# Performance work log

Hardware: AMD Instinct MI355X
Metric: run time of the kernel (lower is better)

## Reference

```python
import jax, jax.numpy as jnp
import numpy as np

NUM_CENTROIDS = 2048
EMA_DECAY = 0.99
GAMMA = 1.0
EPS = 1e-08


def setup_inputs() -> dict:
    key = jax.random.key(0)
    k1, k2 = jax.random.split(key)
    B, T, D = 32, 512, 512
    inputs = jax.random.normal(k1, (B, T, D), dtype=jnp.float32)
    # variance_scaling(0.1, 'fan_avg', 'normal') init for the codebook
    fan_avg = (NUM_CENTROIDS + D) / 2.0
    std = np.sqrt(0.1 / fan_avg).astype(np.float32)
    codebook = jax.random.normal(k2, (NUM_CENTROIDS, D), dtype=jnp.float32) * std
    cluster_counts = jnp.ones((NUM_CENTROIDS,), dtype=jnp.float32)
    return {"inputs": inputs, "codebook": codebook,
            "cluster_counts": cluster_counts, "train": 1}


def reference(inputs, codebook, cluster_counts, train):
    D = inputs.shape[-1]
    K = codebook.shape[0]
    flat = jnp.reshape(inputs, (-1, D))  # [N, D]

    # similarity of stop-gradient features to codebook rows: [N, K]
    features = jax.lax.stop_gradient(flat)
    similarity = jnp.einsum('nd,kd->nk', features, codebook)
    scores = jax.nn.softmax(similarity, axis=-1)
    nn_idx = jnp.argmax(scores, axis=-1)  # [N]

    # cluster counts = column sums of one-hot encodings -> scatter-add
    counts = jnp.zeros((K,), dtype=scores.dtype).at[nn_idx].add(1.0)
    if train:
        new_counts = EMA_DECAY * cluster_counts + (1.0 - EMA_DECAY) * counts
    else:
        new_counts = cluster_counts

    # one_hot @ codebook == gather of codebook rows
    quantized = codebook[nn_idx]  # [N, D]
    quantized = quantized - jnp.mean(quantized, axis=-1, keepdims=True)
    quantized = quantized / jnp.linalg.norm(quantized, axis=-1, keepdims=True)
    quantized = jnp.reshape(quantized, inputs.shape)

    # entropy-based quantization loss (scalar), broadcast to [..., K]
    h_clust = -jnp.mean(jnp.sum(scores * jnp.log2(scores + EPS), axis=-1))
    diversity = jnp.mean(scores, axis=0)
    h_diversity = -jnp.sum(diversity * jnp.log2(diversity + EPS))
    loss = h_clust - GAMMA * h_diversity
    quantization_loss = jnp.full(inputs.shape[:-1] + (K,), loss)

    # straight-through estimator
    quantized = inputs + jax.lax.stop_gradient(quantized - inputs)

    nn_idx_out = jnp.reshape(nn_idx, inputs.shape[:-1])[None]  # [1, B, T]
    codebook_values = jax.lax.stop_gradient(codebook)[None]     # [1, K, D]
    return (quantized, quantization_loss, nn_idx_out, codebook_values, new_counts)
```

## Files before the change

### kernel.cpp

```cpp
#include <hip/hip_runtime.h>
#include <cstddef>
#include <cmath>

#define NROWS 16384
#define DIM   512
#define KC    2048

#define Q_OFF    0ul
#define LOSS_OFF 8388608ul
#define NN_OFF   41943040ul
#define CB_OFF   41959424ul
#define CNT_OFF  43008000ul

#define ENT_OFF  4194304ul

#define FLAG_CAP 4096
#define FLAG_TAU 3e-5f

#define WS_LOSS   0
#define WS_CNT    4
#define WS_NFLAG  3076
#define WS_FLAGS  3080
#define WS_DIVLOG 15376

typedef __attribute__((ext_vector_type(8))) short short8;
typedef __attribute__((ext_vector_type(4))) float f32x4;

__device__ __forceinline__ short hi1(float f) {
    return (short)(__float_as_uint(f) >> 16);
}
__device__ __forceinline__ short lo1(float f) {
    unsigned int u = __float_as_uint(f);
    float l = f - __uint_as_float(u & 0xffff0000u);
    return (short)(__float_as_uint(l) >> 16);
}
__device__ __forceinline__ short8 hi8(float4 a, float4 b) {
    short8 r;
    r[0]=hi1(a.x); r[1]=hi1(a.y); r[2]=hi1(a.z); r[3]=hi1(a.w);
    r[4]=hi1(b.x); r[5]=hi1(b.y); r[6]=hi1(b.z); r[7]=hi1(b.w);
    return r;
}
__device__ __forceinline__ short8 lo8(float4 a, float4 b) {
    short8 r;
    r[0]=lo1(a.x); r[1]=lo1(a.y); r[2]=lo1(a.z); r[3]=lo1(a.w);
    r[4]=lo1(b.x); r[5]=lo1(b.y); r[6]=lo1(b.z); r[7]=lo1(b.w);
    return r;
}

__global__ __launch_bounds__(256) void convsplit(const float* __restrict__ x,
                                                 const float* __restrict__ cb,
                                                 ushort* __restrict__ ah,
                                                 ushort* __restrict__ al,
                                                 ushort* __restrict__ bh,
                                                 ushort* __restrict__ bl,
                                                 int* __restrict__ ws) {
    if (blockIdx.x == 0) {
        for (int j = threadIdx.x + WS_CNT; j < WS_CNT + 2048; j += 256) ws[j] = 0;
        if (threadIdx.x == 0) ws[WS_NFLAG] = 0;
    }
    size_t i = (size_t)blockIdx.x * 256 + threadIdx.x;
    const float* src; ushort* dh; ushort* dl; size_t off;
    if (i < 1048576ul) {
        src = x;  dh = ah; dl = al; off = i * 8;
    } else {
        src = cb; dh = bh; dl = bl; off = (i - 1048576ul) * 8;
    }
    float4 a = *(const float4*)(src + off);
    float4 b = *(const float4*)(src + off + 4);
    *(short8*)(dh + off) = hi8(a, b);
    *(short8*)(dl + off) = lo8(a, b);
}

#define P_AH 0
#define P_AL 8192
#define P_BH 16384
#define P_BL 24576
#define BUFS 32768

__global__ __launch_bounds__(512, 2) void gemm_mfma(const ushort* __restrict__ Ah,
                                                    const ushort* __restrict__ Al,
                                                    const ushort* __restrict__ Bh,
                                                    const ushort* __restrict__ Bl,
                                                    float* __restrict__ C) {
    __shared__ ushort smem[65536];
    const int t    = threadIdx.x;
    const int n0   = blockIdx.x * 256;
    const int m0   = blockIdx.y * 256;
    const int lane = t & 63, quad = lane >> 4, lr = lane & 15;
    const int w = t >> 6, wm = w >> 2, wn = w & 3;
    const int wb = w * 1024;

    f32x4 acc[8][4] = {};

    const int srow = w * 32 + (lane >> 2);
    const int gc   = (((lane & 3) ^ ((lane >> 3) & 3)) << 3);

    const ushort* gAh0 = Ah + (size_t)(m0 + srow) * DIM + gc;
    const ushort* gAh1 = gAh0 + 16 * DIM;
    const ushort* gAl0 = Al + (size_t)(m0 + srow) * DIM + gc;
    const ushort* gAl1 = gAl0 + 16 * DIM;
    const ushort* gBh0 = Bh + (size_t)(n0 + srow) * DIM + gc;
    const ushort* gBh1 = gBh0 + 16 * DIM;
    const ushort* gBl0 = Bl + (size_t)(n0 + srow) * DIM + gc;
    const ushort* gBl1 = gBl0 + 16 * DIM;

    const int swz   = ((quad ^ ((lr >> 1) & 3)) << 3);
    const int raOff = (wm * 128 + lr) * 32 + swz;
    const int rbOff = (wn * 64  + lr) * 32 + swz;

    #define GLD16(G, LOFF)                                                          \
        __builtin_amdgcn_global_load_lds(                                           \
            (const __attribute__((address_space(1))) unsigned int*)(G),             \
            (__attribute__((address_space(3))) unsigned int*)(smem + (LOFF)), 16, 0, 0)

    GLD16(gAh0, P_AH + wb);
    GLD16(gAh1, P_AH + wb + 512);
    GLD16(gBh0, P_BH + wb);
    GLD16(gBh1, P_BH + wb + 512);
    GLD16(gAl0, P_AL + wb);
    GLD16(gAl1, P_AL + wb + 512);
    GLD16(gBl0, P_BL + wb);
    GLD16(gBl1, P_BL + wb + 512);
    asm volatile("s_waitcnt vmcnt(4)" ::: "memory");
    __builtin_amdgcn_s_barrier();
    __builtin_amdgcn_sched_barrier(0);

    short8 ah[8], bb[4], al[8], bl[4];

    #pragma unroll 1
    for (int kk = 0; kk < 15; ++kk) {
        const int cb  = (kk & 1) * BUFS;
        const int nb  = cb ^ BUFS;
        const int k0n = (kk + 1) * 32;

        #pragma unroll
        for (int mt = 0; mt < 8; ++mt) ah[mt] = *(const short8*)(smem + cb + P_AH + raOff + mt * 512);
        #pragma unroll
        for (int nt = 0; nt < 4; ++nt) bb[nt] = *(const short8*)(smem + cb + P_BH + rbOff + nt * 512);
        GLD16(gAh0 + k0n, nb + P_AH + wb);
        GLD16(gAh1 + k0n, nb + P_AH + wb + 512);
        GLD16(gBh0 + k0n, nb + P_BH + wb);
        asm volatile("s_waitcnt vmcnt(5)" ::: "memory");
        __builtin_amdgcn_s_barrier();
        __builtin_amdgcn_sched_barrier(0);
        __builtin_amdgcn_s_setprio(1);
        #pragma unroll
        for (int mt = 0; mt < 8; ++mt)
            #pragma unroll
            for (int nt = 0; nt < 4; ++nt)
                acc[mt][nt] = __builtin_amdgcn_mfma_f32_16x16x32_bf16(ah[mt], bb[nt], acc[mt][nt], 0, 0, 0);
        __builtin_amdgcn_s_setprio(0);
        __builtin_amdgcn_s_barrier();
        __builtin_amdgcn_sched_barrier(0);

        #pragma unroll
        for (int mt = 0; mt < 8; ++mt) al[mt] = *(const short8*)(smem + cb + P_AL + raOff + mt * 512);
        GLD16(gBh1 + k0n, nb + P_BH + wb + 512);
        GLD16(gAl0 + k0n, nb + P_AL + wb);
        GLD16(gAl1 + k0n, nb + P_AL + wb + 512);
        asm volatile("s_waitcnt vmcnt(6)" ::: "memory");
        __builtin_amdgcn_s_barrier();
        __builtin_amdgcn_sched_barrier(0);
        __builtin_amdgcn_s_setprio(1);
        #pragma unroll
        for (int mt = 0; mt < 8; ++mt)
            #pragma unroll
            for (int nt = 0; nt < 4; ++nt)
                acc[mt][nt] = __builtin_amdgcn_mfma_f32_16x16x32_bf16(al[mt], bb[nt], acc[mt][nt], 0, 0, 0);
        __builtin_amdgcn_s_setprio(0);
        __builtin_amdgcn_s_barrier();
        __builtin_amdgcn_sched_barrier(0);

        #pragma unroll
        for (int nt = 0; nt < 4; ++nt) bl[nt] = *(const short8*)(smem + cb + P_BL + rbOff + nt * 512);
        GLD16(gBl0 + k0n, nb + P_BL + wb);
        GLD16(gBl1 + k0n, nb + P_BL + wb + 512);
        asm volatile("s_waitcnt vmcnt(4)" ::: "memory");
        __builtin_amdgcn_s_barrier();
        __builtin_amdgcn_sched_barrier(0);
        __builtin_amdgcn_s_setprio(1);
        #pragma unroll
        for (int mt = 0; mt < 8; ++mt)
            #pragma unroll
            for (int nt = 0; nt < 4; ++nt)
                acc[mt][nt] = __builtin_amdgcn_mfma_f32_16x16x32_bf16(ah[mt], bl[nt], acc[mt][nt], 0, 0, 0);
        __builtin_amdgcn_s_setprio(0);
        __builtin_amdgcn_s_barrier();
        __builtin_amdgcn_sched_barrier(0);
    }

    {
        const int cb = BUFS;
        #pragma unroll
        for (int mt = 0; mt < 8; ++mt) ah[mt] = *(const short8*)(smem + cb + P_AH + raOff + mt * 512);
        #pragma unroll
        for (int nt = 0; nt < 4; ++nt) bb[nt] = *(const short8*)(smem + cb + P_BH + rbOff + nt * 512);
        asm volatile("s_waitcnt vmcnt(2)" ::: "memory");
        __builtin_amdgcn_s_barrier();
        __builtin_amdgcn_sched_barrier(0);
        #pragma unroll
        for (int mt = 0; mt < 8; ++mt)
            #pragma unroll
            for (int nt = 0; nt < 4; ++nt)
                acc[mt][nt] = __builtin_amdgcn_mfma_f32_16x16x32_bf16(ah[mt], bb[nt], acc[mt][nt], 0, 0, 0);
        __builtin_amdgcn_s_barrier();
        __builtin_amdgcn_sched_barrier(0);

        #pragma unroll
        for (int mt = 0; mt < 8; ++mt) al[mt] = *(const short8*)(smem + cb + P_AL + raOff + mt * 512);
        asm volatile("s_waitcnt vmcnt(0)" ::: "memory");
        __builtin_amdgcn_s_barrier();
        __builtin_amdgcn_sched_barrier(0);
        #pragma unroll
        for (int mt = 0; mt < 8; ++mt)
            #pragma unroll
            for (int nt = 0; nt < 4; ++nt)
                acc[mt][nt] = __builtin_amdgcn_mfma_f32_16x16x32_bf16(al[mt], bb[nt], acc[mt][nt], 0, 0, 0);
        __builtin_amdgcn_s_barrier();
        __builtin_amdgcn_sched_barrier(0);

        #pragma unroll
        for (int nt = 0; nt < 4; ++nt) bl[nt] = *(const short8*)(smem + cb + P_BL + rbOff + nt * 512);
        #pragma unroll
        for (int mt = 0; mt < 8; ++mt)
            #pragma unroll
            for (int nt = 0; nt < 4; ++nt)
                acc[mt][nt] = __builtin_amdgcn_mfma_f32_16x16x32_bf16(ah[mt], bl[nt], acc[mt][nt], 0, 0, 0);
    }
    #undef GLD16

    #pragma unroll
    for (int mt = 0; mt < 8; ++mt) {
        #pragma unroll
        for (int nt = 0; nt < 4; ++nt) {
            const int r0 = m0 + wm * 128 + mt * 16 + quad * 4;
            const int c0 = n0 + wn * 64 + nt * 16 + lr;
            #pragma unroll
            for (int j = 0; j < 4; ++j)
                C[(size_t)(r0 + j) * KC + c0] = acc[mt][nt][j];
        }
    }
}

__device__ __forceinline__ float block_reduce_sum(float v, volatile float* sf,
                                                  int lane, int w) {
    #pragma unroll
    for (int off = 32; off; off >>= 1) v += __shfl_xor(v, off, 64);
    if (lane == 0) sf[w] = v;
    __syncthreads();
    v = sf[0] + sf[1] + sf[2] + sf[3];
    __syncthreads();
    return v;
}

__global__ __launch_bounds__(256, 4) void rowpass(const float* __restrict__ sim,
                                                  float* __restrict__ nn,
                                                  float* __restrict__ divpart2,
                                                  int*   __restrict__ counts,
                                                  float* __restrict__ entpart,
                                                  int*   __restrict__ nflag,
                                                  int*   __restrict__ flags) {
    __shared__ float divp[KC];
    __shared__ float sent[4];
    const int t = threadIdx.x, lane = t & 63, w = t >> 6;
    const int b = blockIdx.x;
    const int row0 = b * 8 + w * 2;
    const int col0 = lane << 2;

    float4 dacc[8] = {};
    float ent_acc = 0.f;
    const float* base = sim + (size_t)row0 * KC + col0;

    #pragma unroll 1
    for (int rr = 0; rr < 2; ++rr) {
        float4 cur[8];
        const float* rp = base + (size_t)rr * KC;
        #pragma unroll
        for (int j = 0; j < 8; ++j) cur[j] = *(const float4*)(rp + 256 * j);

        float bv = -3.0e38f, rv = -3.0e38f;
        int   bi = 0x7fffffff, ri = 0x7fffffff;
        #pragma unroll
        for (int j = 0; j < 8; ++j) {
            #pragma unroll
            for (int c = 0; c < 4; ++c) {
                float v = (&cur[j].x)[c];
                int   i = col0 + c + 256 * j;
                if (v > bv || (v == bv && i < bi)) { rv = bv; ri = bi; bv = v; bi = i; }
                else if (v > rv || (v == rv && i < ri)) { rv = v; ri = i; }
            }
        }
        #pragma unroll
        for (int off = 32; off; off >>= 1) {
            float obv = __shfl_xor(bv, off, 64);
            int   obi = __shfl_xor(bi, off, 64);
            float orv = __shfl_xor(rv, off, 64);
            int   ori = __shfl_xor(ri, off, 64);
            bool ob = (obv > bv) || (obv == bv && obi < bi);
            float c1v = ob ? bv : obv;  int c1i = ob ? bi : obi;
            float c2v = ob ? orv : rv;  int c2i = ob ? ori : ri;
            bv = ob ? obv : bv;  bi = ob ? obi : bi;
            bool rb = (c1v > c2v) || (c1v == c2v && c1i < c2i);
            rv = rb ? c1v : c2v;  ri = rb ? c1i : c2i;
        }
        const float m = bv;

        float Z = 0.f, S = 0.f;
        #pragma unroll
        for (int j = 0; j < 8; ++j) {
            #pragma unroll
            for (int c = 0; c < 4; ++c) {
                float d = (&cur[j].x)[c] - m;
                float e = expf(d);
                Z += e; S += e * d;
                (&cur[j].x)[c] = e;
            }
        }
        #pragma unroll
        for (int off = 32; off; off >>= 1) {
            Z += __shfl_xor(Z, off, 64);
            S += __shfl_xor(S, off, 64);
        }
        const float inv = 1.0f / Z;
        #pragma unroll
        for (int j = 0; j < 8; ++j) {
            dacc[j].x += cur[j].x * inv; dacc[j].y += cur[j].y * inv;
            dacc[j].z += cur[j].z * inv; dacc[j].w += cur[j].w * inv;
        }

        if (lane == 0) {
            ent_acc += 1.4426950408889634f * (S * inv) - log2f(Z) + 2.9546393e-5f;
            atomicAdd(&counts[bi], 1);
            nn[row0 + rr] = (float)bi;
            if (bv - rv < FLAG_TAU) {
                int e = atomicAdd(nflag, 1);
                if (e < FLAG_CAP) {
                    flags[3*e] = row0 + rr; flags[3*e+1] = bi; flags[3*e+2] = ri;
                }
            }
        }
    }

    if (lane == 0) sent[w] = ent_acc;
    for (int ww = 0; ww < 4; ++ww) {
        if (w == ww) {
            #pragma unroll
            for (int j = 0; j < 8; ++j) {
                float4* p = (float4*)&divp[col0 + 256 * j];
                if (ww == 0) *p = dacc[j];
                else {
                    float4 v = *p;
                    v.x += dacc[j].x; v.y += dacc[j].y;
                    v.z += dacc[j].z; v.w += dacc[j].w;
                    *p = v;
                }
            }
        }
        __syncthreads();
    }
    float4* dst = (float4*)(divpart2 + (size_t)b * KC);
    dst[t]       = *(float4*)&divp[t * 4];
    dst[t + 256] = *(float4*)&divp[t * 4 + 1024];
    if (t == 0) entpart[b] = sent[0] + sent[1] + sent[2] + sent[3];
}

__global__ __launch_bounds__(256) void fixfin(const float* __restrict__ divpart2,
                                              float* __restrict__ part2,
                                              const float* __restrict__ A,
                                              const float* __restrict__ B,
                                              float* __restrict__ nn,
                                              int*   __restrict__ counts,
                                              const int* __restrict__ flags,
                                              const int* __restrict__ nflagp) {
    const int t = threadIdx.x;
    if (blockIdx.x < 128) {
        const int b = blockIdx.x;
        const float* dp = divpart2 + (size_t)b * 16 * KC;
        #pragma unroll
        for (int j = 0; j < 8; ++j) {
            int c = t + 256 * j;
            float s = 0.f;
            #pragma unroll
            for (int r = 0; r < 16; ++r) s += dp[(size_t)r * KC + c];
            part2[(size_t)b * KC + c] = s;
        }
    } else {
        __shared__ float sf[4];
        int nf = *nflagp; if (nf > FLAG_CAP) nf = FLAG_CAP;
        const int lane = t & 63, w = t >> 6;
        for (int e = blockIdx.x - 128; e < nf; e += 128) {
            const int row = flags[3*e], i1 = flags[3*e+1], i2 = flags[3*e+2];
            const float* ar = A + (size_t)row * DIM;
            const float* b1 = B + (size_t)i1 * DIM;
            const float* b2 = B + (size_t)i2 * DIM;
            float d1 = ar[t] * b1[t] + ar[t + 256] * b1[t + 256];
            float d2 = ar[t] * b2[t] + ar[t + 256] * b2[t + 256];
            d1 = block_reduce_sum(d1, sf, lane, w);
            d2 = block_reduce_sum(d2, sf, lane, w);
            if (t == 0 && (d2 > d1 || (d2 == d1 && i2 < i1))) {
                nn[row] = (float)i2;
                atomicSub(&counts[i1], 1);
                atomicAdd(&counts[i2], 1);
            }
            __syncthreads();
        }
    }
}

__global__ __launch_bounds__(256) void fin1b(const float* __restrict__ part2,
                                             float* __restrict__ divlog8) {
    __shared__ float sf[4];
    const int t = threadIdx.x, lane = t & 63, w = t >> 6;
    const int c = blockIdx.x * 256 + t;
    float s = 0.f;
    for (int r = 0; r < 128; ++r) s += part2[(size_t)r * KC + c];
    float d = s * (1.0f / 16384.0f);
    float v = d * log2f(d + 1e-8f);
    float S = block_reduce_sum(v, sf, lane, w);
    if (t == 0) divlog8[blockIdx.x] = S;
}

__global__ __launch_bounds__(256) void fin2(const float* __restrict__ entpart,
                                            const float* __restrict__ divlog8,
                                            float* __restrict__ lossp) {
    __shared__ float sf[4];
    const int t = threadIdx.x, lane = t & 63, w = t >> 6;
    float se = 0.f;
    #pragma unroll
    for (int k = 0; k < 8; ++k) se += entpart[t + 256 * k];
    float Se = block_reduce_sum(se, sf, lane, w);
    float Sd = block_reduce_sum((t < 8) ? divlog8[t] : 0.f, sf, lane, w);
    if (t == 0)
        lossp[0] = (float)(-(double)Se / 16384.0 + (double)Sd);
}

__global__ __launch_bounds__(256) void tail(const float* __restrict__ x,
                                            const float* __restrict__ cb,
                                            const float* __restrict__ oldc,
                                            const int*   __restrict__ counts,
                                            const float* __restrict__ lossp,
                                            const int*   __restrict__ train,
                                            const float* __restrict__ nn,
                                            float* __restrict__ out) {
    const int bb = blockIdx.x;
    const int t  = threadIdx.x;
    if (bb < 4096) {
        const int lane = t & 63;
        const int row  = (bb << 2) + (t >> 6);
        const int idx  = (int)nn[row];
        const float* c  = cb + (size_t)idx * DIM;
        const float* xr = x  + (size_t)row * DIM;

        float4 q0 = *(const float4*)(c + lane * 8);
        float4 q1 = *(const float4*)(c + lane * 8 + 4);

        float s = q0.x+q0.y+q0.z+q0.w + q1.x+q1.y+q1.z+q1.w;
        #pragma unroll
        for (int off = 32; off; off >>= 1) s += __shfl_xor(s, off, 64);
        const float mean = s * (1.0f / 512.0f);
        q0.x -= mean; q0.y -= mean; q0.z -= mean; q0.w -= mean;
        q1.x -= mean; q1.y -= mean; q1.z -= mean; q1.w -= mean;

        float ss = q0.x*q0.x+q0.y*q0.y+q0.z*q0.z+q0.w*q0.w
                 + q1.x*q1.x+q1.y*q1.y+q1.z*q1.z+q1.w*q1.w;
        #pragma unroll
        for (int off = 32; off; off >>= 1) ss += __shfl_xor(ss, off, 64);
        const float inv = 1.0f / sqrtf(ss);

        float4 x0 = *(const float4*)(xr + lane * 8);
        float4 x1 = *(const float4*)(xr + lane * 8 + 4);
        float4 o0, o1;
        o0.x = x0.x + (q0.x*inv - x0.x); o0.y = x0.y + (q0.y*inv - x0.y);
        o0.z = x0.z + (q0.z*inv - x0.z); o0.w = x0.w + (q0.w*inv - x0.w);
        o1.x = x1.x + (q1.x*inv - x1.x); o1.y = x1.y + (q1.y*inv - x1.y);
        o1.z = x1.z + (q1.z*inv - x1.z); o1.w = x1.w + (q1.w*inv - x1.w);
        *(float4*)(out + (size_t)row * DIM + lane * 8)     = o0;
        *(float4*)(out + (size_t)row * DIM + lane * 8 + 4) = o1;
    } else {
        const int bb2 = bb - 4096;
        if (bb2 < 8192) {
            const float l = lossp[0];
            const float4 v = make_float4(l, l, l, l);
            float4* lo = (float4*)(out + LOSS_OFF);
            size_t base4 = (size_t)bb2 * 1024 + t;
            lo[base4]       = v;
            lo[base4 + 256] = v;
            lo[base4 + 512] = v;
            lo[base4 + 768] = v;
        } else if (bb2 < 8192 + 1024) {
            size_t j = (size_t)(bb2 - 8192) * 256 + t;
            ((float4*)(out + CB_OFF))[j] = ((const float4*)cb)[j];
        } else {
            int k = (bb2 - 9216) * 256 + t;
            float nc = train[0] ? 0.99f * oldc[k] + 0.01f * (float)counts[k]
                                : oldc[k];
            out[CNT_OFF + k] = nc;
        }
    }
}

extern "C" void kernel_launch(void* const* d_in, const int* in_sizes, int n_in,
                              void* d_out, int out_size, void* d_ws, size_t ws_size,
                              hipStream_t stream) {
    const float* x     = (const float*)d_in[0];
    const float* cb    = (const float*)d_in[1];
    const float* oldc  = (const float*)d_in[2];
    const int*   train = (const int*)d_in[3];
    float* out = (float*)d_out;

    float* sim      = out + LOSS_OFF;
    float* divpart2 = out + Q_OFF;
    float* entpart  = out + Q_OFF + ENT_OFF;
    float* part2    = out + CB_OFF;
    float* nn       = out + NN_OFF;

    ushort* Ah = (ushort*)(out + Q_OFF);
    ushort* Al = Ah + 8388608ul;
    ushort* Bh = (ushort*)(out + CB_OFF);
    ushort* Bl = Bh + 1048576ul;

    float* lossp   = (float*)d_ws + WS_LOSS;
    int*   counts  = (int*)d_ws   + WS_CNT;
    int*   nflag   = (int*)d_ws   + WS_NFLAG;
    int*   flags   = (int*)d_ws   + WS_FLAGS;
    float* divlog8 = (float*)d_ws + WS_DIVLOG;

    convsplit<<<4608, 256, 0, stream>>>(x, cb, Ah, Al, Bh, Bl, (int*)d_ws);
    gemm_mfma<<<dim3(KC / 256, NROWS / 256), 512, 0, stream>>>(Ah, Al, Bh, Bl, sim);
    rowpass<<<2048, 256, 0, stream>>>(sim, nn, divpart2, counts, entpart, nflag, flags);
    fixfin<<<256, 256, 0, stream>>>(divpart2, part2, x, cb, nn, counts, flags, nflag);
    fin1b<<<8, 256, 0, stream>>>(part2, divlog8);
    fin2<<<1, 256, 0, stream>>>(entpart, divlog8, lossp);
    tail<<<4096 + 9224, 256, 0, stream>>>(x, cb, oldc, counts, lossp, train, nn, out);
}
```

Before: 354.1 us.

## Restructure GEMM k-loop to issue full next-stage prefetch then one barrier per step

Replaces the three-phase interleaved prefetch/compute schedule, which had a barrier between each phase, with a simpler double-buffered loop. Each iteration issues all eight async global-to-LDS loads for the next k-step, waits for the current buffer, runs one barrier, reads all fragments, and then runs all three MFMA groups back to back. The intent is to cut barrier count and sync overhead per k-step and to fold the peeled final iteration into the loop. In exchange, global loads are no longer interleaved with the MFMA groups inside a step, more fragment registers are live at once, and a trailing barrier is still needed before the buffer is reused.

```diff
diff --git a/kernel.cpp b/kernel.cpp
--- a/kernel.cpp
+++ b/kernel.cpp
@@ -113,72 +113,57 @@
             (const __attribute__((address_space(1))) unsigned int*)(G),             \
             (__attribute__((address_space(3))) unsigned int*)(smem + (LOFF)), 16, 0, 0)
 
-    GLD16(gAh0, P_AH + wb);
-    GLD16(gAh1, P_AH + wb + 512);
-    GLD16(gBh0, P_BH + wb);
-    GLD16(gBh1, P_BH + wb + 512);
-    GLD16(gAl0, P_AL + wb);
-    GLD16(gAl1, P_AL + wb + 512);
-    GLD16(gBl0, P_BL + wb);
-    GLD16(gBl1, P_BL + wb + 512);
-    asm volatile("s_waitcnt vmcnt(4)" ::: "memory");
-    __builtin_amdgcn_s_barrier();
-    __builtin_amdgcn_sched_barrier(0);
+    #define ISSUE8(k0v, nbv)                                                        \
+        do {                                                                        \
+            GLD16(gAh0 + (k0v), (nbv) + P_AH + wb);                                 \
+            GLD16(gAh1 + (k0v), (nbv) + P_AH + wb + 512);                           \
+            GLD16(gBh0 + (k0v), (nbv) + P_BH + wb);                                 \
+            GLD16(gBh1 + (k0v), (nbv) + P_BH + wb + 512);                           \
+            GLD16(gAl0 + (k0v), (nbv) + P_AL + wb);                                 \
+            GLD16(gAl1 + (k0v), (nbv) + P_AL + wb + 512);                           \
+            GLD16(gBl0 + (k0v), (nbv) + P_BL + wb);                                 \
+            GLD16(gBl1 + (k0v), (nbv) + P_BL + wb + 512);                           \
+        } while (0)
+
+    ISSUE8(0, 0);
 
     short8 ah[8], bb[4], al[8], bl[4];
 
     #pragma unroll 1
-    for (int kk = 0; kk < 15; ++kk) {
-        const int cb  = (kk & 1) * BUFS;
-        const int nb  = cb ^ BUFS;
-        const int k0n = (kk + 1) * 32;
-
-        #pragma unroll
-        for (int mt = 0; mt < 8; ++mt) ah[mt] = *(const short8*)(smem + cb + P_AH + raOff + mt * 512);
-        #pragma unroll
-        for (int nt = 0; nt < 4; ++nt) bb[nt] = *(const short8*)(smem + cb + P_BH + rbOff + nt * 512);
-        GLD16(gAh0 + k0n, nb + P_AH + wb);
-        GLD16(gAh1 + k0n, nb + P_AH + wb + 512);
-        GLD16(gBh0 + k0n, nb + P_BH + wb);
-        asm volatile("s_waitcnt vmcnt(5)" ::: "memory");
+    for (int kk = 0; kk < 16; ++kk) {
+        const int cb = (kk & 1) * BUFS;
+
+        if (kk < 15) {
+            const int nb  = cb ^ BUFS;
+            const int k0n = (kk + 1) * 32;
+            ISSUE8(k0n, nb);
+            asm volatile("s_waitcnt vmcnt(8)" ::: "memory");
+        } else {
+            asm volatile("s_waitcnt vmcnt(0)" ::: "memory");
+        }
         __builtin_amdgcn_s_barrier();
         __builtin_amdgcn_sched_barrier(0);
+
+        #pragma unroll
+        for (int mt = 0; mt < 8; ++mt) ah[mt] = *(const short8*)(smem + cb + P_AH + raOff + mt * 512);
+        #pragma unroll
+        for (int nt = 0; nt < 4; ++nt) bb[nt] = *(const short8*)(smem + cb + P_BH + rbOff + nt * 512);
+        #pragma unroll
+        for (int mt = 0; mt < 8; ++mt) al[mt] = *(const short8*)(smem + cb + P_AL + raOff + mt * 512);
+        #pragma unroll
+        for (int nt = 0; nt < 4; ++nt) bl[nt] = *(const short8*)(smem + cb + P_BL + rbOff + nt * 512);
+
         __builtin_amdgcn_s_setprio(1);
         #pragma unroll
         for (int mt = 0; mt < 8; ++mt)
             #pragma unroll
             for (int nt = 0; nt < 4; ++nt)
                 acc[mt][nt] = __builtin_amdgcn_mfma_f32_16x16x32_bf16(ah[mt], bb[nt], acc[mt][nt], 0, 0, 0);
-        __builtin_amdgcn_s_setprio(0);
-        __builtin_amdgcn_s_barrier();
-        __builtin_amdgcn_sched_barrier(0);
-
-        #pragma unroll
-        for (int mt = 0; mt < 8; ++mt) al[mt] = *(const short8*)(smem + cb + P_AL + raOff + mt * 512);
-        GLD16(gBh1 + k0n, nb + P_BH + wb + 512);
-        GLD16(gAl0 + k0n, nb + P_AL + wb);
-        GLD16(gAl1 + k0n, nb + P_AL + wb + 512);
-        asm volatile("s_waitcnt vmcnt(6)" ::: "memory");
-        __builtin_amdgcn_s_barrier();
-        __builtin_amdgcn_sched_barrier(0);
-        __builtin_amdgcn_s_setprio(1);
         #pragma unroll
         for (int mt = 0; mt < 8; ++mt)
             #pragma unroll
             for (int nt = 0; nt < 4; ++nt)
                 acc[mt][nt] = __builtin_amdgcn_mfma_f32_16x16x32_bf16(al[mt], bb[nt], acc[mt][nt], 0, 0, 0);
-        __builtin_amdgcn_s_setprio(0);
-        __builtin_amdgcn_s_barrier();
-        __builtin_amdgcn_sched_barrier(0);
-
-        #pragma unroll
-        for (int nt = 0; nt < 4; ++nt) bl[nt] = *(const short8*)(smem + cb + P_BL + rbOff + nt * 512);
-        GLD16(gBl0 + k0n, nb + P_BL + wb);
-        GLD16(gBl1 + k0n, nb + P_BL + wb + 512);
-        asm volatile("s_waitcnt vmcnt(4)" ::: "memory");
-        __builtin_amdgcn_s_barrier();
-        __builtin_amdgcn_sched_barrier(0);
-        __builtin_amdgcn_s_setprio(1);
         #pragma unroll
         for (int mt = 0; mt < 8; ++mt)
             #pragma unroll
@@ -188,45 +173,7 @@
         __builtin_amdgcn_s_barrier();
         __builtin_amdgcn_sched_barrier(0);
     }
-
-    {
-        const int cb = BUFS;
-        #pragma unroll
-        for (int mt = 0; mt < 8; ++mt) ah[mt] = *(const short8*)(smem + cb + P_AH + raOff + mt * 512);
-        #pragma unroll
-        for (int nt = 0; nt < 4; ++nt) bb[nt] = *(const short8*)(smem + cb + P_BH + rbOff + nt * 512);
-        asm volatile("s_waitcnt vmcnt(2)" ::: "memory");
-        __builtin_amdgcn_s_barrier();
-        __builtin_amdgcn_sched_barrier(0);
-        #pragma unroll
-        for (int mt = 0; mt < 8; ++mt)
-            #pragma unroll
-            for (int nt = 0; nt < 4; ++nt)
-                acc[mt][nt] = __builtin_amdgcn_mfma_f32_16x16x32_bf16(ah[mt], bb[nt], acc[mt][nt], 0, 0, 0);
-        __builtin_amdgcn_s_barrier();
-        __builtin_amdgcn_sched_barrier(0);
-
-        #pragma unroll
-        for (int mt = 0; mt < 8; ++mt) al[mt] = *(const short8*)(smem + cb + P_AL + raOff + mt * 512);
-        asm volatile("s_waitcnt vmcnt(0)" ::: "memory");
-        __builtin_amdgcn_s_barrier();
-        __builtin_amdgcn_sched_barrier(0);
-        #pragma unroll
-        for (int mt = 0; mt < 8; ++mt)
-            #pragma unroll
-            for (int nt = 0; nt < 4; ++nt)
-                acc[mt][nt] = __builtin_amdgcn_mfma_f32_16x16x32_bf16(al[mt], bb[nt], acc[mt][nt], 0, 0, 0);
-        __builtin_amdgcn_s_barrier();
-        __builtin_amdgcn_sched_barrier(0);
-
-        #pragma unroll
-        for (int nt = 0; nt < 4; ++nt) bl[nt] = *(const short8*)(smem + cb + P_BL + rbOff + nt * 512);
-        #pragma unroll
-        for (int mt = 0; mt < 8; ++mt)
-            #pragma unroll
-            for (int nt = 0; nt < 4; ++nt)
-                acc[mt][nt] = __builtin_amdgcn_mfma_f32_16x16x32_bf16(ah[mt], bl[nt], acc[mt][nt], 0, 0, 0);
-    }
+    #undef ISSUE8
     #undef GLD16
 
     #pragma unroll
```

After: 364.3 us. 2.9% more time.

## Restructure split-bf16 GEMM main loop into finer interleaved load/MFMA phases

Applied to the files above, without the earlier changes.

Reorganizes the double-buffered split-precision (hi/lo bf16) GEMM loop so that each K step waits and barriers once at the top. Global-to-LDS prefetches are then spread across half-tile MFMA groups, with LDS fragment reads interleaved between them. The peeled final iteration is folded into the loop through a prefetch predicate, and the number of barriers per step drops from six to three. The aim is better overlap of memory traffic with MFMA work and less synchronization stall. The risks are the hand-tuned vmcnt counts and reduced barrier protection on buffer reuse, which could cause correctness or ordering issues.

```diff
diff --git a/kernel.cpp b/kernel.cpp
--- a/kernel.cpp
+++ b/kernel.cpp
@@ -121,111 +121,93 @@
     GLD16(gAl1, P_AL + wb + 512);
     GLD16(gBl0, P_BL + wb);
     GLD16(gBl1, P_BL + wb + 512);
-    asm volatile("s_waitcnt vmcnt(4)" ::: "memory");
-    __builtin_amdgcn_s_barrier();
-    __builtin_amdgcn_sched_barrier(0);
 
     short8 ah[8], bb[4], al[8], bl[4];
 
     #pragma unroll 1
-    for (int kk = 0; kk < 15; ++kk) {
+    for (int kk = 0; kk < 16; ++kk) {
         const int cb  = (kk & 1) * BUFS;
         const int nb  = cb ^ BUFS;
         const int k0n = (kk + 1) * 32;
-
-        #pragma unroll
-        for (int mt = 0; mt < 8; ++mt) ah[mt] = *(const short8*)(smem + cb + P_AH + raOff + mt * 512);
-        #pragma unroll
-        for (int nt = 0; nt < 4; ++nt) bb[nt] = *(const short8*)(smem + cb + P_BH + rbOff + nt * 512);
-        GLD16(gAh0 + k0n, nb + P_AH + wb);
-        GLD16(gAh1 + k0n, nb + P_AH + wb + 512);
-        GLD16(gBh0 + k0n, nb + P_BH + wb);
-        asm volatile("s_waitcnt vmcnt(5)" ::: "memory");
+        const bool pf = (kk < 15);
+
+        asm volatile("s_waitcnt vmcnt(4)" ::: "memory");
         __builtin_amdgcn_s_barrier();
         __builtin_amdgcn_sched_barrier(0);
+
+        if (pf) { GLD16(gAh0 + k0n, nb + P_AH + wb); GLD16(gAh1 + k0n, nb + P_AH + wb + 512); }
+        #pragma unroll
+        for (int mt = 0; mt < 4; ++mt) ah[mt] = *(const short8*)(smem + cb + P_AH + raOff + mt * 512);
+        #pragma unroll
+        for (int nt = 0; nt < 4; ++nt) bb[nt] = *(const short8*)(smem + cb + P_BH + rbOff + nt * 512);
         __builtin_amdgcn_s_setprio(1);
         #pragma unroll
-        for (int mt = 0; mt < 8; ++mt)
+        for (int mt = 0; mt < 4; ++mt)
             #pragma unroll
             for (int nt = 0; nt < 4; ++nt)
                 acc[mt][nt] = __builtin_amdgcn_mfma_f32_16x16x32_bf16(ah[mt], bb[nt], acc[mt][nt], 0, 0, 0);
         __builtin_amdgcn_s_setprio(0);
+
+        if (pf) { GLD16(gBh0 + k0n, nb + P_BH + wb); GLD16(gBh1 + k0n, nb + P_BH + wb + 512); }
+        #pragma unroll
+        for (int mt = 4; mt < 8; ++mt) ah[mt] = *(const short8*)(smem + cb + P_AH + raOff + mt * 512);
+        __builtin_amdgcn_s_setprio(1);
+        #pragma unroll
+        for (int mt = 4; mt < 8; ++mt)
+            #pragma unroll
+            for (int nt = 0; nt < 4; ++nt)
+                acc[mt][nt] = __builtin_amdgcn_mfma_f32_16x16x32_bf16(ah[mt], bb[nt], acc[mt][nt], 0, 0, 0);
+        __builtin_amdgcn_s_setprio(0);
+
+        if (pf) { asm volatile("s_waitcnt vmcnt(6)" ::: "memory"); }
+        else    { asm volatile("s_waitcnt vmcnt(2)" ::: "memory"); }
         __builtin_amdgcn_s_barrier();
         __builtin_amdgcn_sched_barrier(0);
 
-        #pragma unroll
-        for (int mt = 0; mt < 8; ++mt) al[mt] = *(const short8*)(smem + cb + P_AL + raOff + mt * 512);
-        GLD16(gBh1 + k0n, nb + P_BH + wb + 512);
-        GLD16(gAl0 + k0n, nb + P_AL + wb);
-        GLD16(gAl1 + k0n, nb + P_AL + wb + 512);
-        asm volatile("s_waitcnt vmcnt(6)" ::: "memory");
-        __builtin_amdgcn_s_barrier();
-        __builtin_amdgcn_sched_barrier(0);
+        if (pf) { GLD16(gAl0 + k0n, nb + P_AL + wb); GLD16(gAl1 + k0n, nb + P_AL + wb + 512); }
+        #pragma unroll
+        for (int mt = 0; mt < 4; ++mt) al[mt] = *(const short8*)(smem + cb + P_AL + raOff + mt * 512);
         __builtin_amdgcn_s_setprio(1);
         #pragma unroll
-        for (int mt = 0; mt < 8; ++mt)
+        for (int mt = 0; mt < 4; ++mt)
             #pragma unroll
             for (int nt = 0; nt < 4; ++nt)
                 acc[mt][nt] = __builtin_amdgcn_mfma_f32_16x16x32_bf16(al[mt], bb[nt], acc[mt][nt], 0, 0, 0);
         __builtin_amdgcn_s_setprio(0);
+
+        if (pf) { GLD16(gBl0 + k0n, nb + P_BL + wb); GLD16(gBl1 + k0n, nb + P_BL + wb + 512); }
+        #pragma unroll
+        for (int mt = 4; mt < 8; ++mt) al[mt] = *(const short8*)(smem + cb + P_AL + raOff + mt * 512);
+        __builtin_amdgcn_s_setprio(1);
+        #pragma unroll
+        for (int mt = 4; mt < 8; ++mt)
+            #pragma unroll
+            for (int nt = 0; nt < 4; ++nt)
+                acc[mt][nt] = __builtin_amdgcn_mfma_f32_16x16x32_bf16(al[mt], bb[nt], acc[mt][nt], 0, 0, 0);
+        __builtin_amdgcn_s_setprio(0);
+
+        if (pf) { asm volatile("s_waitcnt vmcnt(8)" ::: "memory"); }
+        else    { asm volatile("s_waitcnt vmcnt(0)" ::: "memory"); }
         __builtin_amdgcn_s_barrier();
         __builtin_amdgcn_sched_barrier(0);
 
         #pragma unroll
         for (int nt = 0; nt < 4; ++nt) bl[nt] = *(const short8*)(smem + cb + P_BL + rbOff + nt * 512);
-        GLD16(gBl0 + k0n, nb + P_BL + wb);
-        GLD16(gBl1 + k0n, nb + P_BL + wb + 512);
-        asm volatile("s_waitcnt vmcnt(4)" ::: "memory");
-        __builtin_amdgcn_s_barrier();
-        __builtin_amdgcn_sched_barrier(0);
         __builtin_amdgcn_s_setprio(1);
         #pragma unroll
-        for (int mt = 0; mt < 8; ++mt)
+        for (int mt = 0; mt < 4; ++mt)
             #pragma unroll
             for (int nt = 0; nt < 4; ++nt)
                 acc[mt][nt] = __builtin_amdgcn_mfma_f32_16x16x32_bf16(ah[mt], bl[nt], acc[mt][nt], 0, 0, 0);
         __builtin_amdgcn_s_setprio(0);
-        __builtin_amdgcn_s_barrier();
-        __builtin_amdgcn_sched_barrier(0);
-    }
-
-    {
-        const int cb = BUFS;
-        #pragma unroll
-        for (int mt = 0; mt < 8; ++mt) ah[mt] = *(const short8*)(smem + cb + P_AH + raOff + mt * 512);
-        #pragma unroll
-        for (int nt = 0; nt < 4; ++nt) bb[nt] = *(const short8*)(smem + cb + P_BH + rbOff + nt * 512);
-        asm volatile("s_waitcnt vmcnt(2)" ::: "memory");
-        __builtin_amdgcn_s_barrier();
-        __builtin_amdgcn_sched_barrier(0);
-        #pragma unroll
-        for (int mt = 0; mt < 8; ++mt)
-            #pragma unroll
-            for (int nt = 0; nt < 4; ++nt)
-                acc[mt][nt] = __builtin_amdgcn_mfma_f32_16x16x32_bf16(ah[mt], bb[nt], acc[mt][nt], 0, 0, 0);
-        __builtin_amdgcn_s_barrier();
-        __builtin_amdgcn_sched_barrier(0);
-
-        #pragma unroll
-        for (int mt = 0; mt < 8; ++mt) al[mt] = *(const short8*)(smem + cb + P_AL + raOff + mt * 512);
-        asm volatile("s_waitcnt vmcnt(0)" ::: "memory");
-        __builtin_amdgcn_s_barrier();
-        __builtin_amdgcn_sched_barrier(0);
-        #pragma unroll
-        for (int mt = 0; mt < 8; ++mt)
-            #pragma unroll
-            for (int nt = 0; nt < 4; ++nt)
-                acc[mt][nt] = __builtin_amdgcn_mfma_f32_16x16x32_bf16(al[mt], bb[nt], acc[mt][nt], 0, 0, 0);
-        __builtin_amdgcn_s_barrier();
-        __builtin_amdgcn_sched_barrier(0);
-
-        #pragma unroll
-        for (int nt = 0; nt < 4; ++nt) bl[nt] = *(const short8*)(smem + cb + P_BL + rbOff + nt * 512);
-        #pragma unroll
-        for (int mt = 0; mt < 8; ++mt)
+
+        __builtin_amdgcn_s_setprio(1);
+        #pragma unroll
+        for (int mt = 4; mt < 8; ++mt)
             #pragma unroll
             for (int nt = 0; nt < 4; ++nt)
                 acc[mt][nt] = __builtin_amdgcn_mfma_f32_16x16x32_bf16(ah[mt], bl[nt], acc[mt][nt], 0, 0, 0);
+        __builtin_amdgcn_s_setprio(0);
     }
     #undef GLD16
 
```

New measurement: 357.8 us, median of 2. No clear change (+1.1%).
